# Performance work log

Hardware: AMD Instinct MI355X
Metric: run time of the kernel (lower is better)

The kernel has to match this reference:

```python
import jax, jax.numpy as jnp
import numpy as np

MATCH_THRESH = 0.5
NEG_POS = 3
VAR0, VAR1 = 0.1, 0.2
THETA = 0.99
NEG_INF = -1e30


def point_form(c):
    # (cx, cy, w, h) -> (x1, y1, x2, y2)
    return jnp.concatenate([c[..., :2] - c[..., 2:] / 2, c[..., :2] + c[..., 2:] / 2], -1)


def iou(a, b):
    # a: [M,4] point form, b: [A,4] point form -> [M,A]
    lt = jnp.maximum(a[:, None, :2], b[None, :, :2])
    rb = jnp.minimum(a[:, None, 2:], b[None, :, 2:])
    wh = jnp.clip(rb - lt, 0.0)
    inter = wh[..., 0] * wh[..., 1]
    area_a = ((a[:, 2] - a[:, 0]) * (a[:, 3] - a[:, 1]))[:, None]
    area_b = ((b[:, 2] - b[:, 0]) * (b[:, 3] - b[:, 1]))[None, :]
    return inter / (area_a + area_b - inter)


def encode(matched, anc):
    # matched: [A,4] point-form matched GT boxes; anc: [A,4] center form
    g_cxcy = ((matched[:, :2] + matched[:, 2:]) * 0.5 - anc[:, :2]) / (VAR0 * anc[:, 2:])
    g_wh = jnp.log((matched[:, 2:] - matched[:, :2]) / anc[:, 2:]) / VAR1
    return jnp.concatenate([g_cxcy, g_wh], -1)


def match(gt_boxes, gt_labels, anc):
    # GuaranteedEncode: SSD bipartite+threshold matching with each GT guaranteed its best anchor
    M = gt_boxes.shape[0]
    ov = iou(gt_boxes, point_form(anc))  # [M, A]
    best_gt_ov = ov.max(0)               # [A]
    best_gt_idx = ov.argmax(0)           # [A]
    best_anchor = ov.argmax(1)           # [M]
    best_gt_ov = best_gt_ov.at[best_anchor].set(2.0)
    best_gt_idx = best_gt_idx.at[best_anchor].set(jnp.arange(M))
    conf = jnp.where(best_gt_ov < MATCH_THRESH, 0, gt_labels[best_gt_idx])
    loc = encode(gt_boxes[best_gt_idx], anc)
    return conf, loc


def decode(loc, anc):
    # apply ARM deltas to anchors; keep center form for re-matching
    cxcy = anc[:, :2] + loc[:, :2] * VAR0 * anc[:, 2:]
    wh = anc[:, 2:] * jnp.exp(loc[:, 2:] * VAR1)
    return jnp.concatenate([cxcy, wh], -1)


def smooth_l1(x):
    a = jnp.abs(x)
    return jnp.where(a < 1.0, 0.5 * a * a, a - 0.5)


def ce_from_logits(logits, labels):
    return -jnp.take_along_axis(jax.nn.log_softmax(logits, -1), labels[..., None], -1)[..., 0]


def setup_inputs():
    key = jax.random.key(0)
    B, A, C, M = 32, 16320, 21, 20
    ks = jax.random.split(key, 8)
    objectness = jax.random.normal(ks[0], (B, A, 2), jnp.float32)
    refine_loc = jax.random.normal(ks[1], (B, A, 4), jnp.float32)
    pred_conf = jax.random.normal(ks[2], (B, A, C), jnp.float32)
    pred_loc = jax.random.normal(ks[3], (B, A, 4), jnp.float32)
    a_cxcy = jax.random.uniform(ks[4], (1, A, 2), jnp.float32, 0.0, 1.0)
    a_wh = jax.random.uniform(ks[5], (1, A, 2), jnp.float32, 0.05, 0.5)
    anchors = jnp.concatenate([a_cxcy, a_wh], -1)  # center form
    g_cxcy = jax.random.uniform(ks[6], (B, M, 2), jnp.float32, 0.15, 0.85)
    g_wh = jax.random.uniform(ks[7], (B, M, 2), jnp.float32, 0.05, 0.3)
    gt_boxes = jnp.concatenate([g_cxcy - g_wh / 2, g_cxcy + g_wh / 2], -1)  # point form
    gt_labels = jax.random.randint(jax.random.fold_in(key, 9), (B, M), 1, C)
    return {"objectness": objectness, "refine_loc": refine_loc, "pred_conf": pred_conf,
            "pred_loc": pred_loc, "anchors": anchors, "gt_boxes": gt_boxes, "gt_labels": gt_labels}


def reference(objectness, refine_loc, pred_conf, pred_loc, anchors, gt_boxes, gt_labels):
    B, A, C = pred_conf.shape
    anc = anchors[0]
    # --- ARM stage: match GTs to fixed anchors ---
    tconf, tloc = jax.vmap(lambda gb, gl: match(gb, gl, anc))(gt_boxes, gt_labels)  # [B,A], [B,A,4]
    pos = tconf > 0
    arm_N = jnp.sum(pos).astype(jnp.float32)
    arm_loc_loss = jnp.sum(smooth_l1(refine_loc - tloc).sum(-1) * pos)
    arm_cls_loss = jnp.sum(ce_from_logits(objectness, pos.astype(jnp.int32)))
    # --- ODM stage: re-match against ARM-refined anchors, filtered by objectness ---
    object_mask = jax.nn.softmax(objectness, -1)[..., 0] < THETA  # [B,A]
    refined = jax.vmap(lambda l: decode(l, anc))(refine_loc)       # [B,A,4] center form
    tconf2, tloc2 = jax.vmap(match)(gt_boxes, gt_labels, refined)
    tloc2 = jax.lax.stop_gradient(tloc2)  # .detach() in the original
    pos2 = (tconf2 > 0) & object_mask
    N = jnp.sum(pos2).astype(jnp.float32)
    loc_loss = jnp.sum(smooth_l1(pred_loc - tloc2).sum(-1) * pos2)
    ce = ce_from_logits(pred_conf, tconf2)  # [B,A]
    pos_num = pos2.sum(-1)                  # [B]
    neg_num = jnp.maximum(10, jnp.minimum(pos_num * NEG_POS, A - pos_num))
    neg_losses = jnp.where(object_mask & (tconf2 == 0), ce, NEG_INF)
    sorted_neg = -jnp.sort(-neg_losses, axis=-1)  # descending: hard-negative mining
    take = (jnp.arange(A)[None, :] < neg_num[:, None]) & (sorted_neg > NEG_INF / 2)
    class_loss = jnp.sum(ce * pos2) + jnp.sum(jnp.where(take, sorted_neg, 0.0))
    class_loss = class_loss / N
    loc_loss = loc_loss / N
    arm_cls_loss = 0.04 * arm_cls_loss / arm_N
    arm_loc_loss = arm_loc_loss / arm_N
    total = class_loss + loc_loss + arm_cls_loss + arm_loc_loss
    return (total, class_loss, loc_loss, arm_cls_loss, arm_loc_loss)
```

## Files before the change

kernel.cpp:

```cpp
#include <hip/hip_runtime.h>
#include <math.h>

#define MATCH_THRESH 0.5f
#define THETA 0.99f
#define NEG_INF_F (-1e30f)


__device__ __forceinline__ float iou_pf(
    float ax1, float ay1, float ax2, float ay2,
    float bx1, float by1, float bx2, float by2) {
  float lx = fmaxf(ax1, bx1), ly = fmaxf(ay1, by1);
  float rx = fminf(ax2, bx2), ry = fminf(ay2, by2);
  float w = fmaxf(rx - lx, 0.f), h = fmaxf(ry - ly, 0.f);
  float inter = w * h;
  float aa = (ax2 - ax1) * (ay2 - ay1);
  float ab = (bx2 - bx1) * (by2 - by1);
  return inter / (aa + ab - inter);
}

__device__ __forceinline__ float sl1(float x) {
  float a = fabsf(x);
  return (a < 1.f) ? 0.5f * a * a : a - 0.5f;
}

__device__ __forceinline__ float wredf(float v) {
#pragma unroll
  for (int o = 32; o > 0; o >>= 1) v += __shfl_down(v, o, 64);
  return v;
}

__device__ __forceinline__ int wredi(int v) {
#pragma unroll
  for (int o = 32; o > 0; o >>= 1) v += __shfl_down(v, o, 64);
  return v;
}

__device__ __forceinline__ unsigned wredmaxu(unsigned v) {
#pragma unroll
  for (int o = 32; o > 0; o >>= 1) {
    unsigned ov = __shfl_down(v, o, 64);
    v = (ov > v) ? ov : v;
  }
  return v;
}

__device__ __forceinline__ unsigned long long wredmax64(unsigned long long v) {
#pragma unroll
  for (int o = 32; o > 0; o >>= 1) {
    unsigned lo = (unsigned)v, hi = (unsigned)(v >> 32);
    unsigned olo = __shfl_down(lo, o, 64);
    unsigned ohi = __shfl_down(hi, o, 64);
    unsigned long long ov = ((unsigned long long)ohi << 32) | olo;
    v = (ov > v) ? ov : v;
  }
  return v;
}

__device__ __forceinline__ unsigned fkey(float v) {
  unsigned b = __float_as_uint(v);
  return (b & 0x80000000u) ? ~b : (b | 0x80000000u);
}
__device__ __forceinline__ float keyf(unsigned u) {
  unsigned b = (u & 0x80000000u) ? (u & 0x7fffffffu) : ~u;
  return __uint_as_float(b);
}


__global__ __launch_bounds__(256) void gt_best_kernel(
    const float* __restrict__ gt_boxes,
    const float4* __restrict__ an4,
    const float4* __restrict__ rl4all,
    unsigned long long* __restrict__ ba1p,
    unsigned long long* __restrict__ ba2p,
    int B, int M, int A) {
  int bm = blockIdx.y;
  int b = bm / M;
  bool refined = (blockIdx.z == 1);
  unsigned long long* dst = refined ? ba2p : ba1p;
  const float4* rl4 = rl4all + (size_t)b * A;
  const float* g = gt_boxes + (size_t)bm * 4;
  float gx1 = g[0], gy1 = g[1], gx2 = g[2], gy2 = g[3];

  int chunk = (A + gridDim.x - 1) / gridDim.x;
  int start = blockIdx.x * chunk;
  int end = min(start + chunk, A);

  unsigned long long best = 0ull;
  for (int a = start + threadIdx.x; a < end; a += blockDim.x) {
    float4 an = an4[a];
    float cx = an.x, cy = an.y, w = an.z, h = an.w;
    if (refined) {
      float4 rl = rl4[a];
      cx += rl.x * 0.1f * w;
      cy += rl.y * 0.1f * h;
      w *= expf(rl.z * 0.2f);
      h *= expf(rl.w * 0.2f);
    }
    float v = iou_pf(gx1, gy1, gx2, gy2,
                     cx - w * 0.5f, cy - h * 0.5f, cx + w * 0.5f, cy + h * 0.5f);
    unsigned long long key =
        ((unsigned long long)fkey(v) << 32) | (unsigned)(~(unsigned)a);
    if (key > best) best = key;
  }
  best = wredmax64(best);
  __shared__ unsigned long long sm[4];
  int w = threadIdx.x >> 6;
  if ((threadIdx.x & 63) == 0) sm[w] = best;
  __syncthreads();
  if (threadIdx.x == 0) {
    unsigned long long m = sm[0];
    for (int i = 1; i < 4; i++) m = (sm[i] > m) ? sm[i] : m;
    atomicMax(&dst[bm], m);
  }
}


template <int CC>
__global__ __launch_bounds__(256) void loss_kernel(
    const float* __restrict__ gt_boxes, const int* __restrict__ gt_labels,
    const float* __restrict__ anchors, const float* __restrict__ refine_loc,
    const float* __restrict__ objectness, const float* __restrict__ pred_conf,
    const float* __restrict__ pred_loc,
    const unsigned long long* __restrict__ ba1p,
    const unsigned long long* __restrict__ ba2p,
    double* __restrict__ accB,
    int* __restrict__ armNB,
    int* __restrict__ poscnt,
    float* __restrict__ negl,
    int B, int M, int A, int C) {
  __shared__ float sgb[128];
  __shared__ int sb1[32], sb2[32], sgl[32];
  __shared__ float sf[4][4];
  __shared__ int sw[2][4];

  int b = blockIdx.y;
  int tid = threadIdx.x;
  if (tid < M) {
    sb1[tid] = (int)(~(unsigned)ba1p[(size_t)b * M + tid]);
    sb2[tid] = (int)(~(unsigned)ba2p[(size_t)b * M + tid]);
    sgl[tid] = gt_labels[(size_t)b * M + tid];
  }
  if (tid < M * 4) sgb[tid] = gt_boxes[(size_t)b * M * 4 + tid];
  __syncthreads();

  float p_arm_loc = 0.f, p_arm_cls = 0.f, p_loc = 0.f, p_cepos = 0.f;
  int p_armN = 0, p_pos2 = 0;

  int stride = gridDim.x * blockDim.x;
#pragma unroll 2
  for (int a = blockIdx.x * blockDim.x + tid; a < A; a += stride) {
    float pr[CC > 0 ? CC : 1];
    const float* pc = pred_conf + ((size_t)b * A + a) * C;
    if constexpr (CC > 0) {
#pragma unroll
      for (int c = 0; c < CC; c++) pr[c] = pc[c];
    }
    float4 an = ((const float4*)anchors)[a];
    float4 rl = ((const float4*)refine_loc)[(size_t)b * A + a];
    float2 ob = ((const float2*)objectness)[(size_t)b * A + a];

    float ax1 = an.x - an.z * 0.5f, ay1 = an.y - an.w * 0.5f;
    float ax2 = an.x + an.z * 0.5f, ay2 = an.y + an.w * 0.5f;
    float rcx = an.x + rl.x * 0.1f * an.z;
    float rcy = an.y + rl.y * 0.1f * an.w;
    float rw = an.z * expf(rl.z * 0.2f);
    float rh = an.w * expf(rl.w * 0.2f);
    float rx1 = rcx - rw * 0.5f, ry1 = rcy - rh * 0.5f;
    float rx2 = rcx + rw * 0.5f, ry2 = rcy + rh * 0.5f;

    float bestA = -1.f, bestR = -1.f;
    int biA = 0, biR = 0;
    for (int m = 0; m < M; m++) {
      float g0 = sgb[m * 4], g1 = sgb[m * 4 + 1], g2 = sgb[m * 4 + 2], g3 = sgb[m * 4 + 3];
      float vA = iou_pf(g0, g1, g2, g3, ax1, ay1, ax2, ay2);
      if (vA > bestA) { bestA = vA; biA = m; }
      float vR = iou_pf(g0, g1, g2, g3, rx1, ry1, rx2, ry2);
      if (vR > bestR) { bestR = vR; biR = m; }
    }
    for (int m = 0; m < M; m++) {
      if (sb1[m] == a) { biA = m; bestA = 2.f; }
      if (sb2[m] == a) { biR = m; bestR = 2.f; }
    }
    int conf1 = (bestA < MATCH_THRESH) ? 0 : sgl[biA];
    int conf2 = (bestR < MATCH_THRESH) ? 0 : sgl[biR];
    int pos1 = conf1 > 0;

    if (pos1) {
      const float* g = sgb + biA * 4;
      float gcx = ((g[0] + g[2]) * 0.5f - an.x) / (0.1f * an.z);
      float gcy = ((g[1] + g[3]) * 0.5f - an.y) / (0.1f * an.w);
      float gw = logf((g[2] - g[0]) / an.z) / 0.2f;
      float gh = logf((g[3] - g[1]) / an.w) / 0.2f;
      p_arm_loc += sl1(rl.x - gcx) + sl1(rl.y - gcy) + sl1(rl.z - gw) + sl1(rl.w - gh);
    }
    float mx = fmaxf(ob.x, ob.y);
    float e0 = expf(ob.x - mx), e1 = expf(ob.y - mx);
    float lse = mx + logf(e0 + e1);
    p_arm_cls += lse - (pos1 ? ob.y : ob.x);
    p_armN += pos1;

    bool mask = (e0 / (e0 + e1)) < THETA;
    int pos2 = (conf2 > 0) && mask;

    float ce;
    if constexpr (CC > 0) {
      float mxc = pr[0];
#pragma unroll
      for (int c = 1; c < CC; c++) mxc = fmaxf(mxc, pr[c]);
      float s = 0.f;
#pragma unroll
      for (int c = 0; c < CC; c++) s += expf(pr[c] - mxc);
      float sel = pr[0];
#pragma unroll
      for (int c = 1; c < CC; c++) sel = (conf2 == c) ? pr[c] : sel;
      ce = mxc + logf(s) - sel;
    } else {
      float mxc = pc[0];
      float s = 1.f;
      for (int c = 1; c < C; c++) {
        float v = pc[c];
        float nm = fmaxf(mxc, v);
        s = s * expf(mxc - nm) + expf(v - nm);
        mxc = nm;
      }
      ce = mxc + logf(s) - pc[conf2];
    }

    if (pos2) {
      const float* g = sgb + biR * 4;
      float gcx = ((g[0] + g[2]) * 0.5f - rcx) / (0.1f * rw);
      float gcy = ((g[1] + g[3]) * 0.5f - rcy) / (0.1f * rh);
      float gw = logf((g[2] - g[0]) / rw) / 0.2f;
      float gh = logf((g[3] - g[1]) / rh) / 0.2f;
      float4 pl = ((const float4*)pred_loc)[(size_t)b * A + a];
      p_loc += sl1(pl.x - gcx) + sl1(pl.y - gcy) + sl1(pl.z - gw) + sl1(pl.w - gh);
      p_cepos += ce;
      p_pos2 += 1;
    }
    negl[(size_t)b * A + a] = (mask && conf2 == 0) ? fmaxf(ce, 0.f) : NEG_INF_F;
  }

  p_arm_loc = wredf(p_arm_loc); p_arm_cls = wredf(p_arm_cls);
  p_loc = wredf(p_loc); p_cepos = wredf(p_cepos);
  p_armN = wredi(p_armN); p_pos2 = wredi(p_pos2);
  int w = tid >> 6;
  if ((tid & 63) == 0) {
    sf[0][w] = p_arm_loc; sf[1][w] = p_arm_cls; sf[2][w] = p_loc; sf[3][w] = p_cepos;
    sw[0][w] = p_armN; sw[1][w] = p_pos2;
  }
  __syncthreads();
  if (tid == 0) {
    float aL = 0, aC = 0, oL = 0, oC = 0;
    int aN = 0, p2 = 0;
    for (int i = 0; i < 4; i++) {
      aL += sf[0][i]; aC += sf[1][i]; oL += sf[2][i]; oC += sf[3][i];
      aN += sw[0][i]; p2 += sw[1][i];
    }
    double* ab = accB + (size_t)b * 8;
    if (aL != 0.f) atomicAdd(&ab[0], (double)aL);
    atomicAdd(&ab[1], (double)aC);
    if (oL != 0.f) atomicAdd(&ab[2], (double)oL);
    if (oC != 0.f) atomicAdd(&ab[3], (double)oC);
    if (aN) atomicAdd(&armNB[b], aN);
    if (p2) atomicAdd(&poscnt[b], p2);
  }
}


__global__ __launch_bounds__(1024) void hardneg_kernel(
    const float* __restrict__ negl, const int* __restrict__ poscnt,
    const double* __restrict__ accB, const int* __restrict__ armNB,
    double* __restrict__ acc4, int* __restrict__ ctr,
    int B, int A, float* __restrict__ out) {
  int b = blockIdx.x;
  const float* nl = negl + (size_t)b * A;
  int t = threadIdx.x;
  unsigned key[16];
#pragma unroll
  for (int j = 0; j < 16; j++) {
    int i = j * 1024 + t;
    key[j] = (i < A) ? fkey(nl[i]) : 0u;
  }
  __shared__ int wcnt[2][16];
  __shared__ float wsum[16];
  __shared__ unsigned wmax[16];
  int w = t >> 6;
  bool lane0 = (t & 63) == 0;

  const unsigned UVALID = fkey(-5e29f);
  int cv = 0;
  unsigned mk = 0;
#pragma unroll
  for (int j = 0; j < 16; j++) {
    cv += (key[j] > UVALID) ? 1 : 0;
    mk = (key[j] > mk) ? key[j] : mk;
  }
  cv = wredi(cv);
  mk = wredmaxu(mk);
  if (lane0) { wcnt[0][w] = cv; wmax[w] = mk; }
  __syncthreads();
  int cnt_valid = 0;
  unsigned maxkey = 0;
  for (int i = 0; i < 16; i++) {
    cnt_valid += wcnt[0][i];
    maxkey = (wmax[i] > maxkey) ? wmax[i] : maxkey;
  }

  int pn = poscnt[b];
  int nn = max(10, min(pn * 3, A - pn));
  int K = min(nn, cnt_valid);

  if (K > 0) {
    unsigned lo = 0x7fffffffu;
    unsigned hi = (maxkey > lo) ? maxkey : lo;
    int par = 1;
    while (lo < hi) {
      unsigned d = hi - lo;
      unsigned mid = lo + (d >> 1) + (d & 1u);
      int c = 0;
#pragma unroll
      for (int j = 0; j < 16; j++) c += (key[j] >= mid) ? 1 : 0;
      c = wredi(c);
      if (lane0) wcnt[par][w] = c;
      __syncthreads();
      int tot = 0;
      for (int i = 0; i < 16; i++) tot += wcnt[par][i];
      par ^= 1;
      if (tot >= K) {
        lo = mid;
        if (tot == K) break;
      } else hi = mid - 1;
    }

    float kth = keyf(lo);
    float sum = 0.f;
    int c1 = 0;
#pragma unroll
    for (int j = 0; j < 16; j++)
      if (key[j] > lo) { sum += keyf(key[j]); c1++; }
    sum = wredf(sum);
    c1 = wredi(c1);
    __syncthreads();
    if (lane0) { wsum[w] = sum; wcnt[0][w] = c1; }
    __syncthreads();
    if (t == 0) {
      float S = 0.f;
      int C1 = 0;
      for (int i = 0; i < 16; i++) { S += wsum[i]; C1 += wcnt[0][i]; }
      S += (float)(K - C1) * kth;
      atomicAdd(acc4, (double)S);
    }
  }

  if (t == 0) {
    __threadfence();
    int old = atomicAdd(ctr, 1);
    if (old == B - 1) {
      __threadfence();
      double arm_loc = 0, arm_cls = 0, odm_loc = 0, ce_pos = 0;
      long long Ni = 0, aNi = 0;
      for (int bb = 0; bb < B; bb++) {
        const double* ab = accB + (size_t)bb * 8;
        arm_loc += ab[0]; arm_cls += ab[1]; odm_loc += ab[2]; ce_pos += ab[3];
        Ni += poscnt[bb]; aNi += armNB[bb];
      }
      double neg_sum = *acc4;
      double N = (double)Ni, armN = (double)aNi;
      double class_loss = (ce_pos + neg_sum) / N;
      double loc_loss = odm_loc / N;
      double acls = 0.04 * arm_cls / armN;
      double aloc = arm_loc / armN;
      out[0] = (float)(class_loss + loc_loss + acls + aloc);
      out[1] = (float)class_loss;
      out[2] = (float)loc_loss;
      out[3] = (float)acls;
      out[4] = (float)aloc;
    }
  }
}


extern "C" void kernel_launch(void* const* d_in, const int* in_sizes, int n_in,
                              void* d_out, int out_size, void* d_ws, size_t ws_size,
                              hipStream_t stream) {
  const float* objectness = (const float*)d_in[0];
  const float* refine_loc = (const float*)d_in[1];
  const float* pred_conf  = (const float*)d_in[2];
  const float* pred_loc   = (const float*)d_in[3];
  const float* anchors    = (const float*)d_in[4];
  const float* gt_boxes   = (const float*)d_in[5];
  const int*   gt_labels  = (const int*)d_in[6];

  int A = in_sizes[4] / 4;
  int B = in_sizes[0] / (A * 2);
  int C = (int)(in_sizes[2] / ((long long)B * A));
  int M = in_sizes[5] / (B * 4);

  char* ws = (char*)d_ws;
  double* acc4 = (double*)ws;
  int* poscnt = (int*)(ws + 64);
  int* armNB = (int*)(ws + 192);
  int* ctr = (int*)(ws + 320);
  double* accB = (double*)(ws + 512);
  size_t ba_off = 512 + (size_t)B * 64;
  unsigned long long* ba1p = (unsigned long long*)(ws + ba_off);
  unsigned long long* ba2p = (unsigned long long*)(ws + ba_off + (size_t)B * M * 8);
  size_t negl_off = ba_off + 2 * (size_t)B * M * 8;
  negl_off = (negl_off + 255) & ~(size_t)255;
  float* negl = (float*)(ws + negl_off);

  hipMemsetAsync(d_ws, 0, negl_off, stream);

  dim3 gbg(4, B * M, 2);
  gt_best_kernel<<<gbg, 256, 0, stream>>>(gt_boxes, (const float4*)anchors,
                                          (const float4*)refine_loc, ba1p, ba2p, B, M, A);

  dim3 grid(16, B);
  if (C == 21) {
    loss_kernel<21><<<grid, 256, 0, stream>>>(gt_boxes, gt_labels, anchors, refine_loc,
                                              objectness, pred_conf, pred_loc, ba1p, ba2p,
                                              accB, armNB, poscnt, negl, B, M, A, C);
  } else {
    loss_kernel<0><<<grid, 256, 0, stream>>>(gt_boxes, gt_labels, anchors, refine_loc,
                                             objectness, pred_conf, pred_loc, ba1p, ba2p,
                                             accB, armNB, poscnt, negl, B, M, A, C);
  }

  hardneg_kernel<<<B, 1024, 0, stream>>>(negl, poscnt, accB, armNB, acc4, ctr,
                                         B, A, (float*)d_out);
}
```

Measured before the change: 113.3 us.

## Fuse per-GT and per-anchor IoU matching into one pass, store anchor bests

Adds a templated match kernel that computes the IoU matrix once per batch and per box set. In that single pass it keeps the per-GT best-anchor keys in registers (reduced with one atomicMax per wave) and writes each anchor's best GT and overlap to workspace. The loss kernel then reads these precomputed values instead of recomputing M IoUs twice, and its grid is doubled. The change removes the redundant IoU work split across B*M blocks, at the cost of extra global traffic for the per-anchor buffers and higher register pressure from 20 live 64-bit keys.

```diff
diff --git a/kernel.cpp b/kernel.cpp
--- a/kernel.cpp
+++ b/kernel.cpp
@@ -66,13 +66,73 @@
 }
 
 
-__global__ __launch_bounds__(256) void gt_best_kernel(
+template <int MM>
+__global__ __launch_bounds__(256) void match_kernel(
     const float* __restrict__ gt_boxes,
     const float4* __restrict__ an4,
     const float4* __restrict__ rl4all,
     unsigned long long* __restrict__ ba1p,
     unsigned long long* __restrict__ ba2p,
-    int B, int M, int A) {
+    unsigned long long* __restrict__ anbA,
+    unsigned long long* __restrict__ anbR,
+    int B, int A) {
+  int b = blockIdx.y;
+  bool refined = (blockIdx.z == 1);
+  unsigned long long* gdst = refined ? ba2p : ba1p;
+  unsigned long long* anb = refined ? anbR : anbA;
+  const float4* rl4 = rl4all + (size_t)b * A;
+
+  __shared__ float sgb[MM * 4];
+  if (threadIdx.x < MM * 4) sgb[threadIdx.x] = gt_boxes[(size_t)b * MM * 4 + threadIdx.x];
+  __syncthreads();
+
+  int chunk = (A + gridDim.x - 1) / gridDim.x;
+  int start = blockIdx.x * chunk;
+  int end = min(start + chunk, A);
+
+  unsigned long long bk[MM];
+#pragma unroll
+  for (int m = 0; m < MM; m++) bk[m] = 0ull;
+
+  for (int a = start + threadIdx.x; a < end; a += blockDim.x) {
+    float4 an = an4[a];
+    float cx = an.x, cy = an.y, w = an.z, h = an.w;
+    if (refined) {
+      float4 rl = rl4[a];
+      cx += rl.x * 0.1f * w;
+      cy += rl.y * 0.1f * h;
+      w *= expf(rl.z * 0.2f);
+      h *= expf(rl.w * 0.2f);
+    }
+    float x1 = cx - w * 0.5f, y1 = cy - h * 0.5f;
+    float x2 = cx + w * 0.5f, y2 = cy + h * 0.5f;
+    float bb = -1.f;
+    int bi = 0;
+    unsigned inva = (unsigned)(~(unsigned)a);
+#pragma unroll
+    for (int m = 0; m < MM; m++) {
+      float v = iou_pf(sgb[m * 4], sgb[m * 4 + 1], sgb[m * 4 + 2], sgb[m * 4 + 3],
+                       x1, y1, x2, y2);
+      if (v > bb) { bb = v; bi = m; }
+      unsigned long long key = ((unsigned long long)fkey(v) << 32) | inva;
+      bk[m] = (key > bk[m]) ? key : bk[m];
+    }
+    anb[(size_t)b * A + a] = ((unsigned long long)fkey(bb) << 32) | (unsigned)bi;
+  }
+
+  bool lane0 = (threadIdx.x & 63) == 0;
+#pragma unroll
+  for (int m = 0; m < MM; m++) {
+    unsigned long long k = wredmax64(bk[m]);
+    if (lane0 && k) atomicMax(&gdst[(size_t)b * MM + m], k);
+  }
+}
+
+
+__global__ __launch_bounds__(256) void gt_best_kernel(
+    const float* __restrict__ gt_boxes, const float4* __restrict__ an4,
+    const float4* __restrict__ rl4all, unsigned long long* __restrict__ ba1p,
+    unsigned long long* __restrict__ ba2p, int B, int M, int A) {
   int bm = blockIdx.y;
   int b = bm / M;
   bool refined = (blockIdx.z == 1);
@@ -115,7 +175,7 @@
 }
 
 
-template <int CC>
+template <int CC, bool PRE>
 __global__ __launch_bounds__(256) void loss_kernel(
     const float* __restrict__ gt_boxes, const int* __restrict__ gt_labels,
     const float* __restrict__ anchors, const float* __restrict__ refine_loc,
@@ -123,6 +183,8 @@
     const float* __restrict__ pred_loc,
     const unsigned long long* __restrict__ ba1p,
     const unsigned long long* __restrict__ ba2p,
+    const unsigned long long* __restrict__ anbA,
+    const unsigned long long* __restrict__ anbR,
     double* __restrict__ accB,
     int* __restrict__ armNB,
     int* __restrict__ poscnt,
@@ -155,27 +217,38 @@
 #pragma unroll
       for (int c = 0; c < CC; c++) pr[c] = pc[c];
     }
+    unsigned long long qa = 0, qr = 0;
+    if constexpr (PRE) {
+      qa = anbA[(size_t)b * A + a];
+      qr = anbR[(size_t)b * A + a];
+    }
     float4 an = ((const float4*)anchors)[a];
     float4 rl = ((const float4*)refine_loc)[(size_t)b * A + a];
     float2 ob = ((const float2*)objectness)[(size_t)b * A + a];
 
-    float ax1 = an.x - an.z * 0.5f, ay1 = an.y - an.w * 0.5f;
-    float ax2 = an.x + an.z * 0.5f, ay2 = an.y + an.w * 0.5f;
     float rcx = an.x + rl.x * 0.1f * an.z;
     float rcy = an.y + rl.y * 0.1f * an.w;
     float rw = an.z * expf(rl.z * 0.2f);
     float rh = an.w * expf(rl.w * 0.2f);
-    float rx1 = rcx - rw * 0.5f, ry1 = rcy - rh * 0.5f;
-    float rx2 = rcx + rw * 0.5f, ry2 = rcy + rh * 0.5f;
-
-    float bestA = -1.f, bestR = -1.f;
-    int biA = 0, biR = 0;
-    for (int m = 0; m < M; m++) {
-      float g0 = sgb[m * 4], g1 = sgb[m * 4 + 1], g2 = sgb[m * 4 + 2], g3 = sgb[m * 4 + 3];
-      float vA = iou_pf(g0, g1, g2, g3, ax1, ay1, ax2, ay2);
-      if (vA > bestA) { bestA = vA; biA = m; }
-      float vR = iou_pf(g0, g1, g2, g3, rx1, ry1, rx2, ry2);
-      if (vR > bestR) { bestR = vR; biR = m; }
+
+    float bestA, bestR;
+    int biA, biR;
+    if constexpr (PRE) {
+      bestA = keyf((unsigned)(qa >> 32)); biA = (int)(unsigned)qa;
+      bestR = keyf((unsigned)(qr >> 32)); biR = (int)(unsigned)qr;
+    } else {
+      float ax1 = an.x - an.z * 0.5f, ay1 = an.y - an.w * 0.5f;
+      float ax2 = an.x + an.z * 0.5f, ay2 = an.y + an.w * 0.5f;
+      float rx1 = rcx - rw * 0.5f, ry1 = rcy - rh * 0.5f;
+      float rx2 = rcx + rw * 0.5f, ry2 = rcy + rh * 0.5f;
+      bestA = -1.f; bestR = -1.f; biA = 0; biR = 0;
+      for (int m = 0; m < M; m++) {
+        float g0 = sgb[m * 4], g1 = sgb[m * 4 + 1], g2 = sgb[m * 4 + 2], g3 = sgb[m * 4 + 3];
+        float vA = iou_pf(g0, g1, g2, g3, ax1, ay1, ax2, ay2);
+        if (vA > bestA) { bestA = vA; biA = m; }
+        float vR = iou_pf(g0, g1, g2, g3, rx1, ry1, rx2, ry2);
+        if (vR > bestR) { bestR = vR; biR = m; }
+      }
     }
     for (int m = 0; m < M; m++) {
       if (sb1[m] == a) { biA = m; bestA = 2.f; }
@@ -405,25 +478,37 @@
   size_t ba_off = 512 + (size_t)B * 64;
   unsigned long long* ba1p = (unsigned long long*)(ws + ba_off);
   unsigned long long* ba2p = (unsigned long long*)(ws + ba_off + (size_t)B * M * 8);
-  size_t negl_off = ba_off + 2 * (size_t)B * M * 8;
-  negl_off = (negl_off + 255) & ~(size_t)255;
+  size_t zero_end = ba_off + 2 * (size_t)B * M * 8;
+
+  size_t anb_off = (zero_end + 255) & ~(size_t)255;
+  size_t fast_negl_off = ((anb_off + 2 * (size_t)B * A * 8) + 255) & ~(size_t)255;
+  size_t fast_need = fast_negl_off + (size_t)B * A * 4;
+  bool fast = (C == 21) && (M == 20) && (B <= 32) && (ws_size >= fast_need);
+
+  unsigned long long* anbA = (unsigned long long*)(ws + anb_off);
+  unsigned long long* anbR = anbA + (size_t)B * A;
+  size_t negl_off = fast ? fast_negl_off : ((zero_end + 255) & ~(size_t)255);
   float* negl = (float*)(ws + negl_off);
 
-  hipMemsetAsync(d_ws, 0, negl_off, stream);
-
-  dim3 gbg(4, B * M, 2);
-  gt_best_kernel<<<gbg, 256, 0, stream>>>(gt_boxes, (const float4*)anchors,
-                                          (const float4*)refine_loc, ba1p, ba2p, B, M, A);
-
-  dim3 grid(16, B);
-  if (C == 21) {
-    loss_kernel<21><<<grid, 256, 0, stream>>>(gt_boxes, gt_labels, anchors, refine_loc,
-                                              objectness, pred_conf, pred_loc, ba1p, ba2p,
-                                              accB, armNB, poscnt, negl, B, M, A, C);
+  hipMemsetAsync(d_ws, 0, zero_end, stream);
+
+  if (fast) {
+    dim3 mg(16, B, 2);
+    match_kernel<20><<<mg, 256, 0, stream>>>(gt_boxes, (const float4*)anchors,
+                                             (const float4*)refine_loc,
+                                             ba1p, ba2p, anbA, anbR, B, A);
+    dim3 grid(32, B);
+    loss_kernel<21, true><<<grid, 256, 0, stream>>>(
+        gt_boxes, gt_labels, anchors, refine_loc, objectness, pred_conf, pred_loc,
+        ba1p, ba2p, anbA, anbR, accB, armNB, poscnt, negl, B, M, A, C);
   } else {
-    loss_kernel<0><<<grid, 256, 0, stream>>>(gt_boxes, gt_labels, anchors, refine_loc,
-                                             objectness, pred_conf, pred_loc, ba1p, ba2p,
-                                             accB, armNB, poscnt, negl, B, M, A, C);
+    dim3 gbg(4, B * M, 2);
+    gt_best_kernel<<<gbg, 256, 0, stream>>>(gt_boxes, (const float4*)anchors,
+                                            (const float4*)refine_loc, ba1p, ba2p, B, M, A);
+    dim3 grid(16, B);
+    loss_kernel<0, false><<<grid, 256, 0, stream>>>(
+        gt_boxes, gt_labels, anchors, refine_loc, objectness, pred_conf, pred_loc,
+        ba1p, ba2p, anbA, anbR, accB, armNB, poscnt, negl, B, M, A, C);
   }
 
   hardneg_kernel<<<B, 1024, 0, stream>>>(negl, poscnt, accB, armNB, acc4, ctr,
```

Result: slower. 118.5 us (+4.6%).
